# Kernel tuning notes

Hardware: AMD Instinct MI355X
Metric: run time of the kernel (lower is better)

Reference implementation:

```python
import jax, jax.numpy as jnp
import numpy as np

N = 50000      # nodes
E = 400000     # edges
IN = 128       # input features
H = 128        # hidden channels
OUT = 64       # output channels
B = 3          # num_blocks
ITERS = 2      # num_iters per block (fix_resistance=True)
EPS = 0.01


def setup_inputs() -> dict:
    key = jax.random.key(0)
    ks = jax.random.split(key, 16)
    g = lambda i, shape, fan_in: jax.random.normal(ks[i], shape, dtype=jnp.float32) * (fan_in ** -0.5)
    return {
        "x": jax.random.normal(ks[0], (N, IN), dtype=jnp.float32),
        "edge_index": jax.random.randint(ks[1], (2, E), 0, N),
        # emb: Linear(IN, H)
        "emb_w": g(2, (H, IN), IN), "emb_b": jnp.zeros((H,), jnp.float32),
        # per-block LaplacianAggr.lin: Linear(H, H, bias=False)
        "lap_w": g(3, (B, H, H), H),
        # per-block edge_resistance_net: Linear(2H, H) -> ReLU -> Linear(H, 1)
        "er_w1": g(4, (B, H, 2 * H), 2 * H), "er_b1": jnp.zeros((B, H), jnp.float32),
        "er_w2": g(5, (B, 1, H), H), "er_b2": jnp.zeros((B, 1), jnp.float32),
        # per-block dissipative_net: Linear(H, H) -> ReLU
        "diss_w": g(6, (B, H, H), H), "diss_b": jnp.zeros((B, H), jnp.float32),
        # per-block mlp: Linear(H,H) -> Tanh -> Linear(H,H)
        "mlp_w1": g(7, (B, H, H), H), "mlp_b1": jnp.zeros((B, H), jnp.float32),
        "mlp_w2": g(8, (B, H, H), H), "mlp_b2": jnp.zeros((B, H), jnp.float32),
        # readout: Linear(H, OUT)
        "ro_w": g(9, (OUT, H), H), "ro_b": jnp.zeros((OUT,), jnp.float32),
    }


def reference(x, edge_index, emb_w, emb_b, lap_w, er_w1, er_b1, er_w2, er_b2,
              diss_w, diss_b, mlp_w1, mlp_b1, mlp_w2, mlp_b2, ro_w, ro_b):
    src, dst = edge_index[0], edge_index[1]
    x = x @ emb_w.T + emb_b                                     # [N, H]
    for b in range(B):
        # edge resistance (fix_resistance=True -> computed once per block)
        ef = jnp.concatenate([x[src], x[dst]], axis=1)          # [E, 2H]
        h = jax.nn.relu(ef @ er_w1[b].T + er_b1[b])             # [E, H]
        r = jnp.abs((h @ er_w2[b].T + er_b2[b])[:, 0])          # [E]
        # get_laplacian(None): L = D - A; deg via scatter at row (src)
        deg = jax.ops.segment_sum(r, src, num_segments=N)       # [N]
        v = jnp.zeros_like(x)
        for _ in range(ITERS):
            f = x @ lap_w[b].T                                  # LaplacianAggr.lin
            # self-loops carry +deg, original edges carry -r, aggregated at dst
            conv = deg[:, None] * f - jax.ops.segment_sum(r[:, None] * f[src], dst, num_segments=N)
            diss = jax.nn.relu(x @ diss_w[b].T + diss_b[b])     # dissipative force
            v = v - EPS * (conv + diss * v)                     # forcing = 0 (NullForce)
            x = x + EPS * v                                     # activ_fun='Identity' inside conv
        x = jnp.tanh(x @ mlp_w1[b].T + mlp_b1[b]) @ mlp_w2[b].T + mlp_b2[b]
    return x @ ro_w.T + ro_b                                    # [N, OUT]
```

## Files before the change

### kernel.cpp

```cpp
#include <hip/hip_runtime.h>
#include <math.h>

constexpr int N_ = 50000;
constexpr int E_ = 400000;
constexpr int H_ = 128;
constexpr int OUT_ = 64;
constexpr int B_ = 3;
constexpr int ITERS_ = 2;
constexpr float EPS_ = 0.01f;

typedef unsigned short u16;
typedef unsigned char u8;
typedef short v8s __attribute__((ext_vector_type(8)));
typedef float v4f __attribute__((ext_vector_type(4)));
typedef float v2f __attribute__((ext_vector_type(2)));

__device__ inline float b2f(u16 u) {
  union { unsigned int i; float f; } c;
  c.i = ((unsigned int)u) << 16;
  return c.f;
}
__device__ inline u16 f2b(float f) {
  union { float f; unsigned int u; } c;
  c.f = f;
  unsigned int r = c.u + 0x7fffu + ((c.u >> 16) & 1u);
  return (u16)(r >> 16);
}
__device__ inline unsigned int pk(float a, float b) {
  return (unsigned int)f2b(a) | ((unsigned int)f2b(b) << 16);
}

#if defined(__has_builtin)
#if __has_builtin(__builtin_nontemporal_load)
#define NT_LOAD(p) __builtin_nontemporal_load(p)
#endif
#endif
#ifndef NT_LOAD
#define NT_LOAD(p) (*(p))
#endif

#if defined(__has_builtin)
#if __has_builtin(__builtin_amdgcn_cvt_pk_f32_fp8) && \
    __has_builtin(__builtin_amdgcn_cvt_pk_fp8_f32)
#define HW_FP8 1
#endif
#endif

#ifdef HW_FP8
__device__ inline v2f dec_lo(unsigned int v) {
  return __builtin_amdgcn_cvt_pk_f32_fp8(v, false);
}
__device__ inline v2f dec_hi(unsigned int v) {
  return __builtin_amdgcn_cvt_pk_f32_fp8(v, true);
}
__device__ inline u8 enc1(float x) {
  return (u8)(__builtin_amdgcn_cvt_pk_fp8_f32(x, x, 0, false) & 0xff);
}
#else
__device__ inline float fp8_dec1(u8 v) {
  const unsigned int s = v >> 7, e = (v >> 3) & 15, m = v & 7;
  float mag = e ? __uint_as_float(((e + 120u) << 23) | (m << 20))
                : (float)m * 0.001953125f;
  return s ? -mag : mag;
}
__device__ inline v2f dec_lo(unsigned int v) {
  v2f r;
  r.x = fp8_dec1((u8)(v & 0xff));
  r.y = fp8_dec1((u8)((v >> 8) & 0xff));
  return r;
}
__device__ inline v2f dec_hi(unsigned int v) {
  v2f r;
  r.x = fp8_dec1((u8)((v >> 16) & 0xff));
  r.y = fp8_dec1((u8)((v >> 24) & 0xff));
  return r;
}
__device__ inline u8 enc1(float x) {
  union { float f; unsigned int u; } c;
  c.f = x;
  const unsigned int sgn = (c.u >> 31) << 7;
  float af = fabsf(x);
  if (af >= 448.f) return (u8)(sgn | 0x7e);
  if (af < 0.015625f) {
    int m = (int)rintf(af * 512.f);
    if (m > 7) return (u8)(sgn | 0x08);
    return (u8)(sgn | m);
  }
  unsigned int u = c.u & 0x7fffffffu;
  u += 0x7ffffu + ((u >> 20) & 1u);
  unsigned int m3 = (u >> 20) & 7;
  int e8 = (int)(u >> 23) - 120;
  if (e8 >= 15 && m3 >= 7) return (u8)(sgn | 0x7e);
  if (e8 <= 0) {
    int m = (int)rintf(af * 512.f);
    if (m > 7) m = 7;
    return (u8)(sgn | m);
  }
  return (u8)(sgn | ((unsigned)e8 << 3) | m3);
}
#endif

template <int CG, int NW, int OT, int A0, int A1, int A2, int A3>
__global__ __launch_bounds__(NW * 64, 1) void gemm_k(
    const u16* __restrict__ Xb, const u16* __restrict__ Wb,
    const float* __restrict__ bias, void* __restrict__ y0,
    void* __restrict__ y1, void* __restrict__ y2, void* __restrict__ y3) {
  constexpr int GW = NW * 32;
  constexpr int ES = (OT == 0) ? 2 : (OT == 1) ? 1 : 4;
  constexpr int DATB = GW * ES;
  constexpr int ROWB = (DATB <= 128) ? 144 : 288;
  constexpr int OSTRIDE = (OT == 0) ? H_ * 2 : (OT == 1) ? H_ : OUT_ * 4;
  __shared__ u8 st[64 * ROWB];

  const int lane = threadIdx.x & 63;
  const int wv = threadIdx.x >> 6;
  const int rowbase = blockIdx.x * 64;
  const int bn = lane & 15;
  const int kc = (lane >> 4) * 8;
  const int ncol = lane & 15;
  const int rsub = (lane >> 4) * 4;

  v8s a[4][4];
#pragma unroll
  for (int rt = 0; rt < 4; ++rt) {
    int arow = rowbase + rt * 16 + bn;
    if (arow >= N_) arow = N_ - 1;
#pragma unroll
    for (int ks = 0; ks < 4; ++ks)
      a[rt][ks] = *(const v8s*)(Xb + (size_t)arow * H_ + ks * 32 + kc);
  }

#pragma unroll
  for (int g = 0; g < CG; ++g) {
    const int cb = g * GW + wv * 32;
    v8s bf[2][4];
#pragma unroll
    for (int ct = 0; ct < 2; ++ct) {
      const u16* wp = Wb + (size_t)(cb + ct * 16 + bn) * H_ + kc;
#pragma unroll
      for (int ks = 0; ks < 4; ++ks) bf[ct][ks] = *(const v8s*)(wp + ks * 32);
    }
    v4f acc[2][4];
#pragma unroll
    for (int ct = 0; ct < 2; ++ct)
#pragma unroll
      for (int rt = 0; rt < 4; ++rt) acc[ct][rt] = (v4f)0.f;
#pragma unroll
    for (int rt = 0; rt < 4; ++rt)
#pragma unroll
      for (int ct = 0; ct < 2; ++ct)
#pragma unroll
        for (int ks = 0; ks < 4; ++ks)
          acc[ct][rt] = __builtin_amdgcn_mfma_f32_16x16x32_bf16(
              a[rt][ks], bf[ct][ks], acc[ct][rt], 0, 0, 0);

    void* yp = (g == 0) ? y0 : (g == 1) ? y1 : (g == 2) ? y2 : y3;
    const int act = (g == 0) ? A0 : (g == 1) ? A1 : (g == 2) ? A2 : A3;
#pragma unroll
    for (int ct = 0; ct < 2; ++ct) {
      const int col = wv * 32 + ct * 16 + ncol;
      const float bv = bias[g * GW + col];
#pragma unroll
      for (int rt = 0; rt < 4; ++rt) {
#pragma unroll
        for (int i = 0; i < 4; ++i) {
          float yv = acc[ct][rt][i] + bv;
          if (act == 1) yv = fmaxf(yv, 0.f);
          if (act == 2) yv = tanhf(yv);
          u8* p = st + (rt * 16 + rsub + i) * ROWB + col * ES;
          if (OT == 0) *(u16*)p = f2b(yv);
          else if (OT == 1) *p = enc1(yv);
          else *(float*)p = yv;
        }
      }
    }
    __syncthreads();
    for (int o = threadIdx.x * 16; o < 64 * DATB; o += NW * 64 * 16) {
      const int row = o / DATB;
      const int cb8 = o - row * DATB;
      const int gr = rowbase + row;
      if (gr < N_)
        *(float4*)((u8*)yp + (size_t)gr * OSTRIDE + cb8) =
            *(const float4*)(st + row * ROWB + cb8);
    }
    if (g + 1 < CG) __syncthreads();
  }
}

__global__ __launch_bounds__(256, 1) void mlp5_k(
    const u16* __restrict__ Xb, const u16* __restrict__ Wm1,
    const float* __restrict__ bm1, const u16* __restrict__ Wm2,
    const float* __restrict__ bm2, u16* __restrict__ Yb) {
  __shared__ u16 tmp[64][144];
  const int lane = threadIdx.x & 63;
  const int wv = threadIdx.x >> 6;
  const int rowbase = blockIdx.x * 64;
  const int cb = wv * 32;
  const int bn = lane & 15;
  const int kc = (lane >> 4) * 8;
  const int ncol = lane & 15;
  const int rsub = (lane >> 4) * 4;

  v8s a[4][4];
#pragma unroll
  for (int rt = 0; rt < 4; ++rt) {
    int arow = rowbase + rt * 16 + bn;
    if (arow >= N_) arow = N_ - 1;
#pragma unroll
    for (int ks = 0; ks < 4; ++ks)
      a[rt][ks] = *(const v8s*)(Xb + (size_t)arow * H_ + ks * 32 + kc);
  }
  v8s bf[2][4];
#pragma unroll
  for (int ct = 0; ct < 2; ++ct) {
    const u16* wp = Wm1 + (size_t)(cb + ct * 16 + bn) * H_ + kc;
#pragma unroll
    for (int ks = 0; ks < 4; ++ks) bf[ct][ks] = *(const v8s*)(wp + ks * 32);
  }
  v4f acc[2][4];
#pragma unroll
  for (int ct = 0; ct < 2; ++ct)
#pragma unroll
    for (int rt = 0; rt < 4; ++rt) acc[ct][rt] = (v4f)0.f;
#pragma unroll
  for (int rt = 0; rt < 4; ++rt)
#pragma unroll
    for (int ct = 0; ct < 2; ++ct)
#pragma unroll
      for (int ks = 0; ks < 4; ++ks)
        acc[ct][rt] = __builtin_amdgcn_mfma_f32_16x16x32_bf16(
            a[rt][ks], bf[ct][ks], acc[ct][rt], 0, 0, 0);
#pragma unroll
  for (int ct = 0; ct < 2; ++ct) {
    const float bv = bm1[cb + ct * 16 + ncol];
#pragma unroll
    for (int rt = 0; rt < 4; ++rt)
#pragma unroll
      for (int i = 0; i < 4; ++i)
        tmp[rt * 16 + rsub + i][cb + ct * 16 + ncol] =
            f2b(tanhf(acc[ct][rt][i] + bv));
  }
  __syncthreads();

#pragma unroll
  for (int rt = 0; rt < 4; ++rt) {
    const int arow = rt * 16 + bn;
#pragma unroll
    for (int ks = 0; ks < 4; ++ks)
      a[rt][ks] = *(const v8s*)&tmp[arow][ks * 32 + kc];
  }
#pragma unroll
  for (int ct = 0; ct < 2; ++ct) {
    const u16* wp = Wm2 + (size_t)(cb + ct * 16 + bn) * H_ + kc;
#pragma unroll
    for (int ks = 0; ks < 4; ++ks) bf[ct][ks] = *(const v8s*)(wp + ks * 32);
  }
  __syncthreads();
#pragma unroll
  for (int ct = 0; ct < 2; ++ct)
#pragma unroll
    for (int rt = 0; rt < 4; ++rt) acc[ct][rt] = (v4f)0.f;
#pragma unroll
  for (int rt = 0; rt < 4; ++rt)
#pragma unroll
    for (int ct = 0; ct < 2; ++ct)
#pragma unroll
      for (int ks = 0; ks < 4; ++ks)
        acc[ct][rt] = __builtin_amdgcn_mfma_f32_16x16x32_bf16(
            a[rt][ks], bf[ct][ks], acc[ct][rt], 0, 0, 0);
#pragma unroll
  for (int ct = 0; ct < 2; ++ct) {
    const float bv = bm2[cb + ct * 16 + ncol];
#pragma unroll
    for (int rt = 0; rt < 4; ++rt)
#pragma unroll
      for (int i = 0; i < 4; ++i)
        tmp[rt * 16 + rsub + i][cb + ct * 16 + ncol] =
            f2b(acc[ct][rt][i] + bv);
  }
  __syncthreads();
  for (int o = threadIdx.x * 16; o < 64 * 256; o += 256 * 16) {
    const int row = o >> 8;
    const int cb8 = o & 255;
    const int gr = rowbase + row;
    if (gr < N_)
      *(float4*)((u8*)Yb + (size_t)gr * (H_ * 2) + cb8) =
          *(const float4*)((const u8*)&tmp[row][0] + cb8);
  }
}

constexpr int WB_EMB = 0;
constexpr int WB_RO = 16384;
constexpr int WB_BLK = 24576;
constexpr int WB_TOTAL = 24576 + 3 * 98304;

__global__ void convall_k(const float* __restrict__ emb_w,
                          const float* __restrict__ ro_w,
                          const float* __restrict__ er_w1,
                          const float* __restrict__ lap_w,
                          const float* __restrict__ diss_w,
                          const float* __restrict__ mlp_w1,
                          const float* __restrict__ mlp_w2,
                          u16* __restrict__ wb) {
  const int idx = blockIdx.x * 256 + threadIdx.x;
  if (idx >= WB_TOTAL) return;
  const float* src;
  size_t soff;
  if (idx < 16384) {
    src = emb_w; soff = idx;
  } else if (idx < 24576) {
    src = ro_w; soff = idx - 16384;
  } else {
    int t = idx - 24576;
    const int b = t / 98304;
    t -= b * 98304;
    if (t < 32768) {
      const int r = t >> 7, c = t & 127;
      src = er_w1 + (size_t)b * 32768;
      soff = (r < 128) ? ((size_t)r * 256 + c) : ((size_t)(r - 128) * 256 + 128 + c);
    } else if (t < 65536) {
      const int u = t - 32768;
      if (u < 16384) { src = lap_w + (size_t)b * 16384; soff = u; }
      else { src = diss_w + (size_t)b * 16384; soff = u - 16384; }
    } else if (t < 81920) {
      src = mlp_w1 + (size_t)b * 16384; soff = t - 65536;
    } else {
      src = mlp_w2 + (size_t)b * 16384; soff = t - 81920;
    }
  }
  wb[idx] = f2b(src[soff]);
}

__global__ void biasp_k(const float* __restrict__ er_b1,
                        const float* __restrict__ diss_b,
                        float* __restrict__ bp512, float* __restrict__ bfd) {
  const int b = blockIdx.x, t = threadIdx.x;
  float v = 0.f;
  if (t < 128) v = er_b1[b * 128 + t];
  else if (t >= 384) v = diss_b[b * 128 + (t - 384)];
  bp512[b * 512 + t] = v;
  if (t < 256) bfd[b * 256 + t] = (t < 128) ? 0.f : diss_b[b * 128 + (t - 128)];
}

__global__ void convx_k(const float* __restrict__ src, u16* __restrict__ dst) {
  const size_t i = ((size_t)blockIdx.x * 256 + threadIdx.x) * 4;
  const float4 v = *(const float4*)(src + i);
  ushort4 o;
  o.x = f2b(v.x); o.y = f2b(v.y); o.z = f2b(v.z); o.w = f2b(v.w);
  *(ushort4*)(dst + i) = o;
}

__global__ __launch_bounds__(256) void edge_r_k(
    const unsigned int* __restrict__ P1, const unsigned int* __restrict__ P2,
    const int* __restrict__ ss, const int* __restrict__ ds,
    const float* __restrict__ w2, const float* __restrict__ b2,
    float* __restrict__ r_out, float* __restrict__ deg) {
  const int tid = threadIdx.x;
  const int lane = tid & 63;
  const int half = lane >> 5;
  const int l = lane & 31;
  const int wid = tid >> 6;
  const size_t e = (size_t)blockIdx.x * 8 + wid * 2 + half;
  const float4 wv = *(const float4*)(w2 + l * 4);
  const int s = ss[e];
  const int d = ds[e];
  const unsigned int a4 = P1[(size_t)s * 32 + l];
  const unsigned int c4 = P2[(size_t)d * 32 + l];
  const v2f alo = dec_lo(a4), ahi = dec_hi(a4);
  const v2f clo = dec_lo(c4), chi = dec_hi(c4);
  float sum = fmaxf(alo.x + clo.x, 0.f) * wv.x;
  sum = fmaf(fmaxf(alo.y + clo.y, 0.f), wv.y, sum);
  sum = fmaf(fmaxf(ahi.x + chi.x, 0.f), wv.z, sum);
  sum = fmaf(fmaxf(ahi.y + chi.y, 0.f), wv.w, sum);
#pragma unroll
  for (int off = 16; off > 0; off >>= 1) sum += __shfl_xor(sum, off);
  if (l == 0) {
    const float rv = fabsf(sum + b2[0]);
    r_out[e] = rv;
    atomicAdd(&deg[s], rv);
  }
}

constexpr int NSC = (N_ + 1023) / 1024;

__global__ void hist_k(const int* __restrict__ dst, int* __restrict__ cnt) {
  const int e = blockIdx.x * 256 + threadIdx.x;
  if (e < E_) atomicAdd(&cnt[dst[e]], 1);
}

__global__ __launch_bounds__(1024) void partial_k(const int* __restrict__ cnt,
                                                  int* __restrict__ psum) {
  __shared__ int sm[1024];
  const int tid = threadIdx.x;
  const int i = blockIdx.x * 1024 + tid;
  sm[tid] = (i < N_) ? cnt[i] : 0;
  __syncthreads();
  for (int off = 512; off > 0; off >>= 1) {
    if (tid < off) sm[tid] += sm[tid + off];
    __syncthreads();
  }
  if (tid == 0) psum[blockIdx.x] = sm[0];
}

__global__ __launch_bounds__(64) void scanp_k(int* __restrict__ psum) {
  const int tid = threadIdx.x;
  int v = (tid < NSC) ? psum[tid] : 0;
  const int orig = v;
#pragma unroll
  for (int off = 1; off < 64; off <<= 1) {
    const int u = __shfl_up(v, off);
    if (tid >= off) v += u;
  }
  if (tid < NSC) psum[tid] = v - orig;
}

__global__ __launch_bounds__(1024) void rowptr_k(const int* __restrict__ cnt,
                                                 const int* __restrict__ psum,
                                                 int* __restrict__ rowptr,
                                                 int* __restrict__ cursor) {
  __shared__ int sm[1024];
  const int tid = threadIdx.x;
  const int i = blockIdx.x * 1024 + tid;
  const int orig = (i < N_) ? cnt[i] : 0;
  sm[tid] = orig;
  __syncthreads();
  for (int off = 1; off < 1024; off <<= 1) {
    const int mine = sm[tid];
    const int u = (tid >= off) ? sm[tid - off] : 0;
    __syncthreads();
    sm[tid] = mine + u;
    __syncthreads();
  }
  const int excl = sm[tid] - orig + psum[blockIdx.x];
  if (i < N_) {
    rowptr[i] = excl;
    cursor[i] = excl;
  }
  if (i == 0) rowptr[N_] = E_;
}

__global__ void permute_k(const int* __restrict__ src,
                          const int* __restrict__ dst, int* __restrict__ cursor,
                          int* __restrict__ ss, int* __restrict__ ds) {
  const int e = blockIdx.x * 256 + threadIdx.x;
  if (e < E_) {
    const int d = dst[e];
    const int p = atomicAdd(&cursor[d], 1);
    ss[p] = src[e];
    ds[p] = d;
  }
}

template <bool FIRST>
__global__ __launch_bounds__(256) void agg_update_k(
    unsigned int* __restrict__ xb, unsigned int* __restrict__ vb,
    const u16* __restrict__ f8, const u16* __restrict__ diss8,
    const float* __restrict__ deg, const float* __restrict__ r,
    const int* __restrict__ ss, const int* __restrict__ rowptr) {
  const int wid = threadIdx.x >> 6;
  const int lane = threadIdx.x & 63;
  const int n = blockIdx.x * 4 + wid;
  const int beg = rowptr[n];
  const int end = rowptr[n + 1];
  float ax = 0.f, ay = 0.f;
  for (int i = beg; i < end; i += 4) {
    const int e1 = (i + 1 < end) ? i + 1 : i;
    const int e2 = (i + 2 < end) ? i + 2 : i;
    const int e3 = (i + 3 < end) ? i + 3 : i;
    const int s0 = NT_LOAD(ss + i);
    const int s1 = NT_LOAD(ss + e1);
    const int s2 = NT_LOAD(ss + e2);
    const int s3 = NT_LOAD(ss + e3);
    const float r0 = NT_LOAD(r + i);
    const float r1 = (i + 1 < end) ? NT_LOAD(r + e1) : 0.f;
    const float r2 = (i + 2 < end) ? NT_LOAD(r + e2) : 0.f;
    const float r3 = (i + 3 < end) ? NT_LOAD(r + e3) : 0.f;
    const unsigned int f0 = f8[(size_t)s0 * 64 + lane];
    const unsigned int f1 = f8[(size_t)s1 * 64 + lane];
    const unsigned int f2 = f8[(size_t)s2 * 64 + lane];
    const unsigned int f3 = f8[(size_t)s3 * 64 + lane];
    const v2f d0 = dec_lo(f0);
    const v2f d1 = dec_lo(f1);
    const v2f d2 = dec_lo(f2);
    const v2f d3 = dec_lo(f3);
    ax = fmaf(r0, d0.x, ax);
    ay = fmaf(r0, d0.y, ay);
    ax = fmaf(r1, d1.x, ax);
    ay = fmaf(r1, d1.y, ay);
    ax = fmaf(r2, d2.x, ax);
    ay = fmaf(r2, d2.y, ay);
    ax = fmaf(r3, d3.x, ax);
    ay = fmaf(r3, d3.y, ay);
  }
  const size_t idx = (size_t)n * 64 + lane;
  const v2f fn = dec_lo((unsigned int)f8[idx]);
  const float dg = deg[n];
  const float cx = dg * fn.x - ax;
  const float cy = dg * fn.y - ay;
  float vx, vy;
  if (FIRST) {
    vx = -EPS_ * cx;
    vy = -EPS_ * cy;
    vb[idx] = pk(vx, vy);
  } else {
    const v2f dsv = dec_lo((unsigned int)diss8[idx]);
    const unsigned int vv = vb[idx];
    vx = b2f((u16)(vv & 0xffffu));
    vy = b2f((u16)(vv >> 16));
    vx = vx - EPS_ * (cx + dsv.x * vx);
    vy = vy - EPS_ * (cy + dsv.y * vy);
  }
  const unsigned int xv = xb[idx];
  const float nx = b2f((u16)(xv & 0xffffu)) + EPS_ * vx;
  const float ny = b2f((u16)(xv >> 16)) + EPS_ * vy;
  xb[idx] = pk(nx, ny);
}

extern "C" void kernel_launch(void* const* d_in, const int* in_sizes, int n_in,
                              void* d_out, int out_size, void* d_ws,
                              size_t ws_size, hipStream_t stream) {
  const float* x_in = (const float*)d_in[0];
  const int* ei = (const int*)d_in[1];
  const int* src = ei;
  const int* dst = ei + E_;
  const float* emb_w = (const float*)d_in[2];
  const float* emb_b = (const float*)d_in[3];
  const float* lap_w = (const float*)d_in[4];
  const float* er_w1 = (const float*)d_in[5];
  const float* er_b1 = (const float*)d_in[6];
  const float* er_w2 = (const float*)d_in[7];
  const float* er_b2 = (const float*)d_in[8];
  const float* diss_w = (const float*)d_in[9];
  const float* diss_b = (const float*)d_in[10];
  const float* mlp_w1 = (const float*)d_in[11];
  const float* mlp_b1 = (const float*)d_in[12];
  const float* mlp_w2 = (const float*)d_in[13];
  const float* mlp_b2 = (const float*)d_in[14];
  const float* ro_w = (const float*)d_in[15];
  const float* ro_b = (const float*)d_in[16];
  float* out = (float*)d_out;

  const size_t NF = (size_t)N_ * H_;
  u16* xb = (u16*)d_ws;
  u16* vb = xb + NF;
  u16* xinb = vb + NF;
  u8* P1 = (u8*)(xinb + NF);
  u8* P2 = P1 + NF;
  u8* F8 = P2 + NF;
  u8* D8 = F8 + NF;
  float* r = (float*)(D8 + NF);
  float* deg = r + E_;
  int* rowptr = (int*)(deg + N_);
  int* cursor = rowptr + (N_ + 1);
  int* ss = cursor + N_;
  int* ds = ss + E_;
  int* psum = ds + E_;
  u16* wb = (u16*)(psum + NSC);
  float* bp512 = (float*)(wb + WB_TOTAL + (WB_TOTAL & 1));
  float* bfd = bp512 + 3 * 512;

  const int g64 = (N_ + 63) / 64;
  const int e_grid = (E_ + 255) / 256;

  convall_k<<<(WB_TOTAL + 255) / 256, 256, 0, stream>>>(
      emb_w, ro_w, er_w1, lap_w, diss_w, mlp_w1, mlp_w2, wb);
  biasp_k<<<3, 512, 0, stream>>>(er_b1, diss_b, bp512, bfd);
  convx_k<<<(int)(NF / 1024), 256, 0, stream>>>(x_in, xinb);

  hipMemsetAsync(cursor, 0, N_ * sizeof(int), stream);
  hist_k<<<e_grid, 256, 0, stream>>>(dst, cursor);
  partial_k<<<NSC, 1024, 0, stream>>>(cursor, psum);
  scanp_k<<<1, 64, 0, stream>>>(psum);
  rowptr_k<<<NSC, 1024, 0, stream>>>(cursor, psum, rowptr, cursor);
  permute_k<<<e_grid, 256, 0, stream>>>(src, dst, cursor, ss, ds);

  gemm_k<1, 4, 0, 0, 0, 0, 0><<<g64, 256, 0, stream>>>(
      xinb, wb + WB_EMB, emb_b, xb, nullptr, nullptr, nullptr);

  for (int b = 0; b < B_; ++b) {
    const u16* Wp = wb + WB_BLK + (size_t)b * 98304;
    const u16* Wfd = Wp + 32768;
    const u16* Wm1 = Wfd + 32768;
    const u16* Wm2 = Wm1 + 16384;
    const float* b2 = er_b2 + b;
    const float* w2 = er_w2 + (size_t)b * H_;

    gemm_k<4, 4, 1, 0, 0, 0, 1><<<g64, 256, 0, stream>>>(
        xb, Wp, bp512 + b * 512, P1, P2, F8, D8);
    hipMemsetAsync(deg, 0, N_ * sizeof(float), stream);
    edge_r_k<<<E_ / 8, 256, 0, stream>>>((const unsigned int*)P1,
                                         (const unsigned int*)P2, ss, ds, w2,
                                         b2, r, deg);

    agg_update_k<true><<<N_ / 4, 256, 0, stream>>>(
        (unsigned int*)xb, (unsigned int*)vb, (const u16*)F8, (const u16*)D8,
        deg, r, ss, rowptr);
    gemm_k<2, 4, 1, 0, 1, 0, 0><<<g64, 256, 0, stream>>>(
        xb, Wfd, bfd + b * 256, F8, D8, nullptr, nullptr);
    agg_update_k<false><<<N_ / 4, 256, 0, stream>>>(
        (unsigned int*)xb, (unsigned int*)vb, (const u16*)F8, (const u16*)D8,
        deg, r, ss, rowptr);

    mlp5_k<<<g64, 256, 0, stream>>>(xb, Wm1, mlp_b1 + b * H_, Wm2,
                                    mlp_b2 + b * H_, xb);
  }
  gemm_k<1, 2, 2, 0, 0, 0, 0><<<g64, 128, 0, stream>>>(
      xb, wb + WB_RO, ro_b, out, nullptr, nullptr, nullptr);
}
```

Measured before the change: 629.4 us.

## Fuse setup kernels, double-buffer GEMM weights/staging, widen edge resistance per thread

Several independent changes. The fp32 input to bf16 conversion is folded into the embedding GEMM, and the bias-packing kernel is merged into the weight-conversion kernel, which removes two launches and one full N×H intermediate. gemm_k now prefetches the next column group's weights and alternates between two shared-memory staging buffers, so the trailing barrier between groups can be dropped. mlp6_k loads both weight matrices up front, and edge_r_k uses 16 lanes per edge with 8-byte loads instead of 32 lanes with 4-byte loads. The cost is more register and shared-memory pressure in the GEMMs.

```diff
diff --git a/kernel.cpp b/kernel.cpp
--- a/kernel.cpp
+++ b/kernel.cpp
@@ -28,6 +28,14 @@
 }
 __device__ inline unsigned int pk(float a, float b) {
   return (unsigned int)f2b(a) | ((unsigned int)f2b(b) << 16);
+}
+__device__ inline v8s pack8(const float4 u, const float4 v) {
+  v8s r;
+  r[0] = (short)f2b(u.x); r[1] = (short)f2b(u.y);
+  r[2] = (short)f2b(u.z); r[3] = (short)f2b(u.w);
+  r[4] = (short)f2b(v.x); r[5] = (short)f2b(v.y);
+  r[6] = (short)f2b(v.z); r[7] = (short)f2b(v.w);
+  return r;
 }
 
 #if defined(__has_builtin)
@@ -100,9 +108,9 @@
 }
 #endif
 
-template <int CG, int NW, int OT, int A0, int A1, int A2, int A3>
+template <int CG, int NW, int AF, int OT, int A0, int A1, int A2, int A3>
 __global__ __launch_bounds__(NW * 64, 1) void gemm_k(
-    const u16* __restrict__ Xb, const u16* __restrict__ Wb,
+    const void* __restrict__ X_, const u16* __restrict__ Wb,
     const float* __restrict__ bias, void* __restrict__ y0,
     void* __restrict__ y1, void* __restrict__ y2, void* __restrict__ y3) {
   constexpr int GW = NW * 32;
@@ -110,7 +118,8 @@
   constexpr int DATB = GW * ES;
   constexpr int ROWB = (DATB <= 128) ? 144 : 288;
   constexpr int OSTRIDE = (OT == 0) ? H_ * 2 : (OT == 1) ? H_ : OUT_ * 4;
-  __shared__ u8 st[64 * ROWB];
+  constexpr int NST = (CG > 1) ? 2 : 1;
+  __shared__ u8 st[NST][64 * ROWB];
 
   const int lane = threadIdx.x & 63;
   const int wv = threadIdx.x >> 6;
@@ -125,20 +134,45 @@
   for (int rt = 0; rt < 4; ++rt) {
     int arow = rowbase + rt * 16 + bn;
     if (arow >= N_) arow = N_ - 1;
-#pragma unroll
-    for (int ks = 0; ks < 4; ++ks)
-      a[rt][ks] = *(const v8s*)(Xb + (size_t)arow * H_ + ks * 32 + kc);
+    if constexpr (AF == 0) {
+      const u16* Xb = (const u16*)X_;
+#pragma unroll
+      for (int ks = 0; ks < 4; ++ks)
+        a[rt][ks] = *(const v8s*)(Xb + (size_t)arow * H_ + ks * 32 + kc);
+    } else {
+      const float* Xf = (const float*)X_;
+#pragma unroll
+      for (int ks = 0; ks < 4; ++ks) {
+        const float4 u =
+            *(const float4*)(Xf + (size_t)arow * H_ + ks * 32 + kc);
+        const float4 v =
+            *(const float4*)(Xf + (size_t)arow * H_ + ks * 32 + kc + 4);
+        a[rt][ks] = pack8(u, v);
+      }
+    }
+  }
+
+  v8s bf0[2][4], bf1[2][4];
+#pragma unroll
+  for (int ct = 0; ct < 2; ++ct) {
+    const u16* wp = Wb + (size_t)(wv * 32 + ct * 16 + bn) * H_ + kc;
+#pragma unroll
+    for (int ks = 0; ks < 4; ++ks) bf0[ct][ks] = *(const v8s*)(wp + ks * 32);
   }
 
 #pragma unroll
   for (int g = 0; g < CG; ++g) {
-    const int cb = g * GW + wv * 32;
-    v8s bf[2][4];
-#pragma unroll
-    for (int ct = 0; ct < 2; ++ct) {
-      const u16* wp = Wb + (size_t)(cb + ct * 16 + bn) * H_ + kc;
-#pragma unroll
-      for (int ks = 0; ks < 4; ++ks) bf[ct][ks] = *(const v8s*)(wp + ks * 32);
+    v8s(*cur)[4] = (g & 1) ? bf1 : bf0;
+    if (g + 1 < CG) {
+      v8s(*nxt)[4] = (g & 1) ? bf0 : bf1;
+#pragma unroll
+      for (int ct = 0; ct < 2; ++ct) {
+        const u16* wp =
+            Wb + (size_t)((g + 1) * GW + wv * 32 + ct * 16 + bn) * H_ + kc;
+#pragma unroll
+        for (int ks = 0; ks < 4; ++ks)
+          nxt[ct][ks] = *(const v8s*)(wp + ks * 32);
+      }
     }
     v4f acc[2][4];
 #pragma unroll
@@ -152,10 +186,10 @@
 #pragma unroll
         for (int ks = 0; ks < 4; ++ks)
           acc[ct][rt] = __builtin_amdgcn_mfma_f32_16x16x32_bf16(
-              a[rt][ks], bf[ct][ks], acc[ct][rt], 0, 0, 0);
-
-    void* yp = (g == 0) ? y0 : (g == 1) ? y1 : (g == 2) ? y2 : y3;
+              a[rt][ks], cur[ct][ks], acc[ct][rt], 0, 0, 0);
+
     const int act = (g == 0) ? A0 : (g == 1) ? A1 : (g == 2) ? A2 : A3;
+    u8* sg = st[g & (NST - 1)];
 #pragma unroll
     for (int ct = 0; ct < 2; ++ct) {
       const int col = wv * 32 + ct * 16 + ncol;
@@ -167,7 +201,7 @@
           float yv = acc[ct][rt][i] + bv;
           if (act == 1) yv = fmaxf(yv, 0.f);
           if (act == 2) yv = tanhf(yv);
-          u8* p = st + (rt * 16 + rsub + i) * ROWB + col * ES;
+          u8* p = sg + (rt * 16 + rsub + i) * ROWB + col * ES;
           if (OT == 0) *(u16*)p = f2b(yv);
           else if (OT == 1) *p = enc1(yv);
           else *(float*)p = yv;
@@ -175,19 +209,19 @@
       }
     }
     __syncthreads();
+    void* yp = (g == 0) ? y0 : (g == 1) ? y1 : (g == 2) ? y2 : y3;
     for (int o = threadIdx.x * 16; o < 64 * DATB; o += NW * 64 * 16) {
       const int row = o / DATB;
       const int cb8 = o - row * DATB;
       const int gr = rowbase + row;
       if (gr < N_)
         *(float4*)((u8*)yp + (size_t)gr * OSTRIDE + cb8) =
-            *(const float4*)(st + row * ROWB + cb8);
+            *(const float4*)(sg + row * ROWB + cb8);
     }
-    if (g + 1 < CG) __syncthreads();
-  }
-}
-
-__global__ __launch_bounds__(256, 1) void mlp5_k(
+  }
+}
+
+__global__ __launch_bounds__(256, 1) void mlp6_k(
     const u16* __restrict__ Xb, const u16* __restrict__ Wm1,
     const float* __restrict__ bm1, const u16* __restrict__ Wm2,
     const float* __restrict__ bm2, u16* __restrict__ Yb) {
@@ -210,13 +244,18 @@
     for (int ks = 0; ks < 4; ++ks)
       a[rt][ks] = *(const v8s*)(Xb + (size_t)arow * H_ + ks * 32 + kc);
   }
-  v8s bf[2][4];
+  v8s bfm1[2][4], bfm2[2][4];
 #pragma unroll
   for (int ct = 0; ct < 2; ++ct) {
-    const u16* wp = Wm1 + (size_t)(cb + ct * 16 + bn) * H_ + kc;
-#pragma unroll
-    for (int ks = 0; ks < 4; ++ks) bf[ct][ks] = *(const v8s*)(wp + ks * 32);
-  }
+    const u16* wp1 = Wm1 + (size_t)(cb + ct * 16 + bn) * H_ + kc;
+    const u16* wp2 = Wm2 + (size_t)(cb + ct * 16 + bn) * H_ + kc;
+#pragma unroll
+    for (int ks = 0; ks < 4; ++ks) {
+      bfm1[ct][ks] = *(const v8s*)(wp1 + ks * 32);
+      bfm2[ct][ks] = *(const v8s*)(wp2 + ks * 32);
+    }
+  }
+
   v4f acc[2][4];
 #pragma unroll
   for (int ct = 0; ct < 2; ++ct)
@@ -229,7 +268,7 @@
 #pragma unroll
       for (int ks = 0; ks < 4; ++ks)
         acc[ct][rt] = __builtin_amdgcn_mfma_f32_16x16x32_bf16(
-            a[rt][ks], bf[ct][ks], acc[ct][rt], 0, 0, 0);
+            a[rt][ks], bfm1[ct][ks], acc[ct][rt], 0, 0, 0);
 #pragma unroll
   for (int ct = 0; ct < 2; ++ct) {
     const float bv = bm1[cb + ct * 16 + ncol];
@@ -249,12 +288,6 @@
     for (int ks = 0; ks < 4; ++ks)
       a[rt][ks] = *(const v8s*)&tmp[arow][ks * 32 + kc];
   }
-#pragma unroll
-  for (int ct = 0; ct < 2; ++ct) {
-    const u16* wp = Wm2 + (size_t)(cb + ct * 16 + bn) * H_ + kc;
-#pragma unroll
-    for (int ks = 0; ks < 4; ++ks) bf[ct][ks] = *(const v8s*)(wp + ks * 32);
-  }
   __syncthreads();
 #pragma unroll
   for (int ct = 0; ct < 2; ++ct)
@@ -267,7 +300,7 @@
 #pragma unroll
       for (int ks = 0; ks < 4; ++ks)
         acc[ct][rt] = __builtin_amdgcn_mfma_f32_16x16x32_bf16(
-            a[rt][ks], bf[ct][ks], acc[ct][rt], 0, 0, 0);
+            a[rt][ks], bfm2[ct][ks], acc[ct][rt], 0, 0, 0);
 #pragma unroll
   for (int ct = 0; ct < 2; ++ct) {
     const float bv = bm2[cb + ct * 16 + ncol];
@@ -293,6 +326,7 @@
 constexpr int WB_RO = 16384;
 constexpr int WB_BLK = 24576;
 constexpr int WB_TOTAL = 24576 + 3 * 98304;
+constexpr int CONV_TOT = WB_TOTAL + 3 * 512 + 3 * 256;
 
 __global__ void convall_k(const float* __restrict__ emb_w,
                           const float* __restrict__ ro_w,
@@ -301,9 +335,27 @@
                           const float* __restrict__ diss_w,
                           const float* __restrict__ mlp_w1,
                           const float* __restrict__ mlp_w2,
-                          u16* __restrict__ wb) {
+                          const float* __restrict__ er_b1,
+                          const float* __restrict__ diss_b,
+                          u16* __restrict__ wb, float* __restrict__ bp512,
+                          float* __restrict__ bfd) {
   const int idx = blockIdx.x * 256 + threadIdx.x;
-  if (idx >= WB_TOTAL) return;
+  if (idx >= CONV_TOT) return;
+  if (idx >= WB_TOTAL) {
+    int t2 = idx - WB_TOTAL;
+    if (t2 < 3 * 512) {
+      const int b = t2 >> 9, t = t2 & 511;
+      float v = 0.f;
+      if (t < 128) v = er_b1[b * 128 + t];
+      else if (t >= 384) v = diss_b[b * 128 + (t - 384)];
+      bp512[b * 512 + t] = v;
+    } else {
+      t2 -= 3 * 512;
+      const int b = t2 >> 8, t = t2 & 255;
+      bfd[b * 256 + t] = (t < 128) ? 0.f : diss_b[b * 128 + (t - 128)];
+    }
+    return;
+  }
   const float* src;
   size_t soff;
   if (idx < 16384) {
@@ -331,50 +383,35 @@
   wb[idx] = f2b(src[soff]);
 }
 
-__global__ void biasp_k(const float* __restrict__ er_b1,
-                        const float* __restrict__ diss_b,
-                        float* __restrict__ bp512, float* __restrict__ bfd) {
-  const int b = blockIdx.x, t = threadIdx.x;
-  float v = 0.f;
-  if (t < 128) v = er_b1[b * 128 + t];
-  else if (t >= 384) v = diss_b[b * 128 + (t - 384)];
-  bp512[b * 512 + t] = v;
-  if (t < 256) bfd[b * 256 + t] = (t < 128) ? 0.f : diss_b[b * 128 + (t - 128)];
-}
-
-__global__ void convx_k(const float* __restrict__ src, u16* __restrict__ dst) {
-  const size_t i = ((size_t)blockIdx.x * 256 + threadIdx.x) * 4;
-  const float4 v = *(const float4*)(src + i);
-  ushort4 o;
-  o.x = f2b(v.x); o.y = f2b(v.y); o.z = f2b(v.z); o.w = f2b(v.w);
-  *(ushort4*)(dst + i) = o;
-}
-
 __global__ __launch_bounds__(256) void edge_r_k(
-    const unsigned int* __restrict__ P1, const unsigned int* __restrict__ P2,
+    const uint2* __restrict__ P1, const uint2* __restrict__ P2,
     const int* __restrict__ ss, const int* __restrict__ ds,
     const float* __restrict__ w2, const float* __restrict__ b2,
     float* __restrict__ r_out, float* __restrict__ deg) {
   const int tid = threadIdx.x;
-  const int lane = tid & 63;
-  const int half = lane >> 5;
-  const int l = lane & 31;
-  const int wid = tid >> 6;
-  const size_t e = (size_t)blockIdx.x * 8 + wid * 2 + half;
-  const float4 wv = *(const float4*)(w2 + l * 4);
+  const int sub = tid & 15;
+  const size_t e = (size_t)blockIdx.x * 16 + (tid >> 4);
+  const float4 w0 = *(const float4*)(w2 + sub * 8);
+  const float4 w1 = *(const float4*)(w2 + sub * 8 + 4);
   const int s = ss[e];
   const int d = ds[e];
-  const unsigned int a4 = P1[(size_t)s * 32 + l];
-  const unsigned int c4 = P2[(size_t)d * 32 + l];
-  const v2f alo = dec_lo(a4), ahi = dec_hi(a4);
-  const v2f clo = dec_lo(c4), chi = dec_hi(c4);
-  float sum = fmaxf(alo.x + clo.x, 0.f) * wv.x;
-  sum = fmaf(fmaxf(alo.y + clo.y, 0.f), wv.y, sum);
-  sum = fmaf(fmaxf(ahi.x + chi.x, 0.f), wv.z, sum);
-  sum = fmaf(fmaxf(ahi.y + chi.y, 0.f), wv.w, sum);
-#pragma unroll
-  for (int off = 16; off > 0; off >>= 1) sum += __shfl_xor(sum, off);
-  if (l == 0) {
+  const uint2 av = P1[(size_t)s * 16 + sub];
+  const uint2 cv = P2[(size_t)d * 16 + sub];
+  const v2f a0 = dec_lo(av.x), a1 = dec_hi(av.x);
+  const v2f a2 = dec_lo(av.y), a3 = dec_hi(av.y);
+  const v2f c0 = dec_lo(cv.x), c1 = dec_hi(cv.x);
+  const v2f c2 = dec_lo(cv.y), c3 = dec_hi(cv.y);
+  float sum = fmaxf(a0.x + c0.x, 0.f) * w0.x;
+  sum = fmaf(fmaxf(a0.y + c0.y, 0.f), w0.y, sum);
+  sum = fmaf(fmaxf(a1.x + c1.x, 0.f), w0.z, sum);
+  sum = fmaf(fmaxf(a1.y + c1.y, 0.f), w0.w, sum);
+  sum = fmaf(fmaxf(a2.x + c2.x, 0.f), w1.x, sum);
+  sum = fmaf(fmaxf(a2.y + c2.y, 0.f), w1.y, sum);
+  sum = fmaf(fmaxf(a3.x + c3.x, 0.f), w1.z, sum);
+  sum = fmaf(fmaxf(a3.y + c3.y, 0.f), w1.w, sum);
+#pragma unroll
+  for (int off = 8; off > 0; off >>= 1) sum += __shfl_xor(sum, off);
+  if (sub == 0) {
     const float rv = fabsf(sum + b2[0]);
     r_out[e] = rv;
     atomicAdd(&deg[s], rv);
@@ -543,8 +580,7 @@
   const size_t NF = (size_t)N_ * H_;
   u16* xb = (u16*)d_ws;
   u16* vb = xb + NF;
-  u16* xinb = vb + NF;
-  u8* P1 = (u8*)(xinb + NF);
+  u8* P1 = (u8*)(vb + NF);
   u8* P2 = P1 + NF;
   u8* F8 = P2 + NF;
   u8* D8 = F8 + NF;
@@ -562,10 +598,9 @@
   const int g64 = (N_ + 63) / 64;
   const int e_grid = (E_ + 255) / 256;
 
-  convall_k<<<(WB_TOTAL + 255) / 256, 256, 0, stream>>>(
-      emb_w, ro_w, er_w1, lap_w, diss_w, mlp_w1, mlp_w2, wb);
-  biasp_k<<<3, 512, 0, stream>>>(er_b1, diss_b, bp512, bfd);
-  convx_k<<<(int)(NF / 1024), 256, 0, stream>>>(x_in, xinb);
+  convall_k<<<(CONV_TOT + 255) / 256, 256, 0, stream>>>(
+      emb_w, ro_w, er_w1, lap_w, diss_w, mlp_w1, mlp_w2, er_b1, diss_b, wb,
+      bp512, bfd);
 
   hipMemsetAsync(cursor, 0, N_ * sizeof(int), stream);
   hist_k<<<e_grid, 256, 0, stream>>>(dst, cursor);
@@ -574,8 +609,8 @@
   rowptr_k<<<NSC, 1024, 0, stream>>>(cursor, psum, rowptr, cursor);
   permute_k<<<e_grid, 256, 0, stream>>>(src, dst, cursor, ss, ds);
 
-  gemm_k<1, 4, 0, 0, 0, 0, 0><<<g64, 256, 0, stream>>>(
-      xinb, wb + WB_EMB, emb_b, xb, nullptr, nullptr, nullptr);
+  gemm_k<1, 4, 1, 0, 0, 0, 0, 0><<<g64, 256, 0, stream>>>(
+      x_in, wb + WB_EMB, emb_b, xb, nullptr, nullptr, nullptr);
 
   for (int b = 0; b < B_; ++b) {
     const u16* Wp = wb + WB_BLK + (size_t)b * 98304;
@@ -585,25 +620,24 @@
     const float* b2 = er_b2 + b;
     const float* w2 = er_w2 + (size_t)b * H_;
 
-    gemm_k<4, 4, 1, 0, 0, 0, 1><<<g64, 256, 0, stream>>>(
+    gemm_k<4, 4, 0, 1, 0, 0, 0, 1><<<g64, 256, 0, stream>>>(
         xb, Wp, bp512 + b * 512, P1, P2, F8, D8);
     hipMemsetAsync(deg, 0, N_ * sizeof(float), stream);
-    edge_r_k<<<E_ / 8, 256, 0, stream>>>((const unsigned int*)P1,
-                                         (const unsigned int*)P2, ss, ds, w2,
-                                         b2, r, deg);
+    edge_r_k<<<E_ / 16, 256, 0, stream>>>((const uint2*)P1, (const uint2*)P2,
+                                          ss, ds, w2, b2, r, deg);
 
     agg_update_k<true><<<N_ / 4, 256, 0, stream>>>(
         (unsigned int*)xb, (unsigned int*)vb, (const u16*)F8, (const u16*)D8,
         deg, r, ss, rowptr);
-    gemm_k<2, 4, 1, 0, 1, 0, 0><<<g64, 256, 0, stream>>>(
+    gemm_k<2, 4, 0, 1, 0, 1, 0, 0><<<g64, 256, 0, stream>>>(
         xb, Wfd, bfd + b * 256, F8, D8, nullptr, nullptr);
     agg_update_k<false><<<N_ / 4, 256, 0, stream>>>(
         (unsigned int*)xb, (unsigned int*)vb, (const u16*)F8, (const u16*)D8,
         deg, r, ss, rowptr);
 
-    mlp5_k<<<g64, 256, 0, stream>>>(xb, Wm1, mlp_b1 + b * H_, Wm2,
+    mlp6_k<<<g64, 256, 0, stream>>>(xb, Wm1, mlp_b1 + b * H_, Wm2,
                                     mlp_b2 + b * H_, xb);
   }
-  gemm_k<1, 2, 2, 0, 0, 0, 0><<<g64, 128, 0, stream>>>(
+  gemm_k<1, 2, 0, 2, 0, 0, 0, 0><<<g64, 128, 0, stream>>>(
       xb, wb + WB_RO, ro_b, out, nullptr, nullptr, nullptr);
 }
```

After: 601.3 us. 1.05x faster.
